# Performance work log

Hardware: AMD Instinct MI355X
Metric: run time of the kernel (lower is better)

The kernel has to match this reference:

```python
import jax, jax.numpy as jnp
import numpy as np

TMSG = 15  # max_len - 1


def setup_inputs() -> dict:
    key = jax.random.key(0)
    ks = jax.random.split(key, 8)
    B, T_in, E, H, V = 4096, 4, 256, 512, 32000
    s = lambda k, shape: jax.random.normal(k, shape, jnp.float32) * 0.05
    return {
        "inp": jax.random.normal(ks[0], (B, T_in, E), jnp.float32),
        "Wx0": s(ks[1], (E, 4 * H)),
        "Wh0": s(ks[2], (H, 4 * H)),
        "b0": jnp.zeros((4 * H,), jnp.float32),
        "Wx1": s(ks[3], (H, 4 * H)),
        "Wh1": s(ks[4], (H, 4 * H)),
        "b1": jnp.zeros((4 * H,), jnp.float32),
        "Wd": s(ks[5], (H, V)),
        "bd": jnp.zeros((V,), jnp.float32),
    }


def _lstm_step(x, h, c, Wx, Wh, b):
    # Keras LSTMCell gate order: i, f, g(cell), o
    z = x @ Wx + h @ Wh + b
    i, f, g, o = jnp.split(z, 4, axis=-1)
    c = jax.nn.sigmoid(f) * c + jax.nn.sigmoid(i) * jnp.tanh(g)
    h = jax.nn.sigmoid(o) * jnp.tanh(c)
    return h, c


def reference(inp, Wx0, Wh0, b0, Wx1, Wh1, b1, Wd, bd):
    B = inp.shape[0]
    H = Wh0.shape[0]
    z = jnp.zeros((B, H), inp.dtype)

    def scan_fn(carry, x_t):
        h0, c0, h1, c1 = carry
        h0, c0 = _lstm_step(x_t, h0, c0, Wx0, Wh0, b0)
        h1, c1 = _lstm_step(h0, h1, c1, Wx1, Wh1, b1)
        return (h0, c0, h1, c1), None

    # NOTE: source bug resets initial_state to None every step, so each of the
    # max_len-1 steps runs the identical stacked LSTM from zero state; we run it once.
    (h0, c0, h1, c1), _ = jax.lax.scan(scan_fn, (z, z, z, z), jnp.swapaxes(inp, 0, 1))
    out = h1  # (B, H) last-step output of top cell

    log_probs = jax.nn.log_softmax(out @ Wd + bd, axis=-1)  # (B, V)
    probs = jnp.exp(log_probs)
    entropy = -jnp.sum(probs * log_probs, axis=-1)  # (B,)

    keys = jax.random.split(jax.random.key(42), TMSG)
    samples = jax.vmap(lambda k: jax.random.categorical(k, log_probs, axis=-1))(keys)  # (T, B)
    lp = log_probs[jnp.arange(B)[None, :], samples]  # (T, B) log_prob of sampled chars
    ent = jnp.broadcast_to(entropy[None], (TMSG, B))  # (T, B)

    message = samples.T  # (B, T)
    message = jnp.concatenate([message, jnp.zeros_like(message)], axis=1)  # (B, 2T)
    state_h = jnp.stack([h0, c0])  # keras unpack quirk: states[0] = [h, c] of cell 0
    return (message, lp, ent, state_h)
```

## Files before the change

### kernel.cpp

```cpp
#include <hip/hip_runtime.h>
#include <stdint.h>
#include <math.h>

#define BB 4096
#define HH 512
#define VV 32000
#define NT 15
#define STF 2097152

struct KeysArg { uint32_t w[2*NT]; };

__host__ __device__ inline void tf2x32(uint32_t k0, uint32_t k1,
                                       uint32_t x0, uint32_t x1,
                                       uint32_t& o0, uint32_t& o1) {
  uint32_t ks2 = k0 ^ k1 ^ 0x1BD11BDAu;
  x0 += k0; x1 += k1;
#define TF_R(r) { x0 += x1; x1 = (x1 << (r)) | (x1 >> (32 - (r))); x1 ^= x0; }
  TF_R(13) TF_R(15) TF_R(26) TF_R(6)
  x0 += k1; x1 += ks2 + 1u;
  TF_R(17) TF_R(29) TF_R(16) TF_R(24)
  x0 += ks2; x1 += k0 + 2u;
  TF_R(13) TF_R(15) TF_R(26) TF_R(6)
  x0 += k0; x1 += k1 + 3u;
  TF_R(17) TF_R(29) TF_R(16) TF_R(24)
  x0 += k1; x1 += ks2 + 4u;
  TF_R(13) TF_R(15) TF_R(26) TF_R(6)
  x0 += ks2; x1 += k0 + 5u;
#undef TF_R
  o0 = x0; o1 = x1;
}

__device__ inline float gumbel32(uint32_t bits) {
  float f = __uint_as_float((bits >> 9) | 0x3f800000u) - 1.0f;
  f = fmaxf(f, 1.17549435e-38f);
  return -logf(-logf(f));
}

__global__ __launch_bounds__(256)
void gemm2_kernel(const float* __restrict__ A1, int lda1, int K1,
                  const float* __restrict__ A2, int lda2, int K2,
                  const float* __restrict__ W1, const float* __restrict__ W2,
                  int ldw,
                  const float* __restrict__ bias,
                  float* __restrict__ C, int ldc)
{
  __shared__ float As[16][128];
  __shared__ float Ws[16][128];
  const int tid = threadIdx.x;
  const int m0 = blockIdx.y * 128;
  const int n0 = blockIdx.x * 128;
  const int tx = tid & 15, ty = tid >> 4;
  float acc[8][8];
  #pragma unroll
  for (int i = 0; i < 8; ++i)
    #pragma unroll
    for (int j = 0; j < 8; ++j) acc[i][j] = 0.0f;

  const int kt1 = K1 >> 4;
  const int kt2 = A2 ? (K2 >> 4) : 0;
  const int sr = tid >> 1, sc = (tid & 1) * 8;
  const int wk = tid >> 4, wn = (tid & 15) * 8;

  for (int kt = 0; kt < kt1 + kt2; ++kt) {
    const float* A; int lda; const float* W; int k0;
    if (kt < kt1) { A = A1; lda = lda1; W = W1; k0 = kt << 4; }
    else          { A = A2; lda = lda2; W = W2; k0 = (kt - kt1) << 4; }
    const float* asrc = A + (size_t)(m0 + sr) * lda + (k0 + sc);
    float4 av0 = *(const float4*)asrc;
    float4 av1 = *(const float4*)(asrc + 4);
    const float* wsrc = W + (size_t)(k0 + wk) * ldw + (n0 + wn);
    float4 wv0 = *(const float4*)wsrc;
    float4 wv1 = *(const float4*)(wsrc + 4);
    As[sc+0][sr]=av0.x; As[sc+1][sr]=av0.y; As[sc+2][sr]=av0.z; As[sc+3][sr]=av0.w;
    As[sc+4][sr]=av1.x; As[sc+5][sr]=av1.y; As[sc+6][sr]=av1.z; As[sc+7][sr]=av1.w;
    *(float4*)&Ws[wk][wn]   = wv0;
    *(float4*)&Ws[wk][wn+4] = wv1;
    __syncthreads();
    #pragma unroll
    for (int kk = 0; kk < 16; ++kk) {
      float4 a0 = *(const float4*)&As[kk][ty*8];
      float4 a1 = *(const float4*)&As[kk][ty*8+4];
      float4 b0 = *(const float4*)&Ws[kk][tx*8];
      float4 b1 = *(const float4*)&Ws[kk][tx*8+4];
      float ar[8] = {a0.x,a0.y,a0.z,a0.w,a1.x,a1.y,a1.z,a1.w};
      float br[8] = {b0.x,b0.y,b0.z,b0.w,b1.x,b1.y,b1.z,b1.w};
      #pragma unroll
      for (int i = 0; i < 8; ++i)
        #pragma unroll
        for (int j = 0; j < 8; ++j)
          acc[i][j] = fmaf(ar[i], br[j], acc[i][j]);
    }
    __syncthreads();
  }
  #pragma unroll
  for (int i = 0; i < 8; ++i) {
    const int m = m0 + ty*8 + i;
    float* dst = C + (size_t)m * ldc + (n0 + tx*8);
    float4 o0, o1;
    o0.x = acc[i][0] + bias[n0+tx*8+0];
    o0.y = acc[i][1] + bias[n0+tx*8+1];
    o0.z = acc[i][2] + bias[n0+tx*8+2];
    o0.w = acc[i][3] + bias[n0+tx*8+3];
    o1.x = acc[i][4] + bias[n0+tx*8+4];
    o1.y = acc[i][5] + bias[n0+tx*8+5];
    o1.z = acc[i][6] + bias[n0+tx*8+6];
    o1.w = acc[i][7] + bias[n0+tx*8+7];
    *(float4*)dst       = o0;
    *(float4*)(dst + 4) = o1;
  }
}

__global__ __launch_bounds__(256)
void gate_kernel(const float* __restrict__ z, const float* __restrict__ cin,
                 float* __restrict__ hout, float* __restrict__ cout,
                 float* __restrict__ sh, float* __restrict__ sc)
{
  int idx = blockIdx.x * 256 + threadIdx.x;
  int b = idx >> 9, j = idx & 511;
  const float* zr = z + (size_t)b * 2048;
  float zi = zr[j], zf = zr[j+512], zg = zr[j+1024], zo = zr[j+1536];
  float si = 1.0f/(1.0f+expf(-zi));
  float sf = 1.0f/(1.0f+expf(-zf));
  float so = 1.0f/(1.0f+expf(-zo));
  float c = sf * cin[idx] + si * tanhf(zg);
  float h = so * tanhf(c);
  cout[idx] = c; hout[idx] = h;
  if (sh) { sh[idx] = h; sc[idx] = c; }
}

__global__ __launch_bounds__(256)
void rowstat_kernel(const float* __restrict__ logits,
                    float* __restrict__ rowM, float* __restrict__ rowLS,
                    float* __restrict__ rowEnt)
{
  const int row = blockIdx.x;
  const float* x = logits + (size_t)row * VV;
  const int tid = threadIdx.x;
  float m = -INFINITY;
  for (int v = tid; v < VV; v += 256) m = fmaxf(m, x[v]);
  #pragma unroll
  for (int off = 32; off; off >>= 1) m = fmaxf(m, __shfl_down(m, off));
  __shared__ float sm[4], ssum[4], swsum[4];
  if ((tid & 63) == 0) sm[tid >> 6] = m;
  __syncthreads();
  m = fmaxf(fmaxf(sm[0], sm[1]), fmaxf(sm[2], sm[3]));
  float s = 0.0f, w = 0.0f;
  for (int v = tid; v < VV; v += 256) {
    float d = x[v] - m;
    float e = expf(d);
    s += e; w += d * e;
  }
  #pragma unroll
  for (int off = 32; off; off >>= 1) { s += __shfl_down(s, off); w += __shfl_down(w, off); }
  if ((tid & 63) == 0) { ssum[tid >> 6] = s; swsum[tid >> 6] = w; }
  __syncthreads();
  if (tid == 0) {
    s = ssum[0]+ssum[1]+ssum[2]+ssum[3];
    w = swsum[0]+swsum[1]+swsum[2]+swsum[3];
    float ls = logf(s);
    rowM[row] = m; rowLS[row] = ls; rowEnt[row] = ls - w / s;
  }
}

__global__ __launch_bounds__(256)
void sample_kernel(const float* __restrict__ logits,
                   const float* __restrict__ rowM, const float* __restrict__ rowLS,
                   const float* __restrict__ rowEnt,
                   float* __restrict__ out,
                   KeysArg keys, int bbase)
{
  const int l = blockIdx.x;
  const int b = bbase + l;
  const float* x = logits + (size_t)l * VV;
  const float m = rowM[l], ls = rowLS[l];

  float bv[NT];
  uint32_t bi[NT];
  #pragma unroll
  for (int t = 0; t < NT; ++t) { bv[t] = -INFINITY; bi[t] = 0; }

  const uint32_t pbase = (uint32_t)b * (uint32_t)VV;
  for (int v = threadIdx.x; v < VV; v += 256) {
    const float lp = (x[v] - m) - ls;
    const uint32_t p = pbase + (uint32_t)v;
    #pragma unroll
    for (int t = 0; t < NT; ++t) {
      uint32_t o0, o1;
      tf2x32(keys.w[2*t], keys.w[2*t+1], 0u, p, o0, o1);
      float g = gumbel32(o0 ^ o1) + lp;
      if (g > bv[t]) { bv[t] = g; bi[t] = (uint32_t)v; }
    }
  }

  __shared__ float rv[NT][4];
  __shared__ uint32_t ri[NT][4];
  const int lane = threadIdx.x & 63, wq = threadIdx.x >> 6;
  #pragma unroll
  for (int t = 0; t < NT; ++t) {
    float v = bv[t]; uint32_t idx = bi[t];
    #pragma unroll
    for (int off = 32; off; off >>= 1) {
      float ov = __shfl_down(v, off);
      uint32_t oi = __shfl_down(idx, off);
      if (ov > v || (ov == v && oi < idx)) { v = ov; idx = oi; }
    }
    if (lane == 0) { rv[t][wq] = v; ri[t][wq] = idx; }
  }
  __syncthreads();
  if (threadIdx.x < NT) {
    const int t = threadIdx.x;
    float v = rv[t][0]; uint32_t idx = ri[t][0];
    #pragma unroll
    for (int q = 1; q < 4; ++q) {
      float ov = rv[t][q]; uint32_t oi = ri[t][q];
      if (ov > v || (ov == v && oi < idx)) { v = ov; idx = oi; }
    }
    out[(size_t)b * 30 + t]      = (float)idx;
    out[(size_t)b * 30 + 15 + t] = 0.0f;
    out[122880 + (size_t)t * BB + b] = (x[idx] - m) - ls;
    out[184320 + (size_t)t * BB + b] = rowEnt[l];
  }
}

extern "C" void kernel_launch(void* const* d_in, const int* in_sizes, int n_in,
                              void* d_out, int out_size, void* d_ws, size_t ws_size,
                              hipStream_t stream)
{
  const float* inp = (const float*)d_in[0];
  const float* Wx0 = (const float*)d_in[1];
  const float* Wh0 = (const float*)d_in[2];
  const float* b0v = (const float*)d_in[3];
  const float* Wx1 = (const float*)d_in[4];
  const float* Wh1 = (const float*)d_in[5];
  const float* b1v = (const float*)d_in[6];
  const float* Wd  = (const float*)d_in[7];
  const float* bdv = (const float*)d_in[8];
  float* out = (float*)d_out;
  float* ws = (float*)d_ws;

  float* h0 = ws;
  float* c0 = ws + (size_t)STF;
  float* h1 = ws + (size_t)2*STF;
  float* c1 = ws + (size_t)3*STF;
  float* z  = ws + (size_t)4*STF;
  float* rowM  = ws + (size_t)8*STF;
  float* rowLS = rowM + 4096;
  float* rowEnt = rowLS + 4096;
  float* logits = ws + (size_t)8*STF + 16384;

  size_t ws_floats = ws_size / 4;
  size_t base = (size_t)8*STF + 16384;
  int CH = 4096;
  while (CH > 128 && base + (size_t)CH*VV > ws_floats) CH >>= 1;

  hipMemsetAsync(ws, 0, (size_t)4*STF*sizeof(float), stream);

  for (int t = 0; t < 4; ++t) {
    gemm2_kernel<<<dim3(2048/128, 4096/128), 256, 0, stream>>>(
        inp + t*256, 1024, 256, h0, 512, 512, Wx0, Wh0, 2048, b0v, z, 2048);
    gate_kernel<<<STF/256, 256, 0, stream>>>(z, c0, h0, c0,
        (t==3) ? out + 245760 : (float*)nullptr,
        (t==3) ? out + 245760 + STF : (float*)nullptr);
    gemm2_kernel<<<dim3(2048/128, 4096/128), 256, 0, stream>>>(
        h0, 512, 512, h1, 512, 512, Wx1, Wh1, 2048, b1v, z, 2048);
    gate_kernel<<<STF/256, 256, 0, stream>>>(z, c1, h1, c1, (float*)nullptr, (float*)nullptr);
  }

  KeysArg ka;
  for (int t = 0; t < NT; ++t) {
    uint32_t o0, o1;
    tf2x32(0u, 42u, 0u, (uint32_t)t, o0, o1);
    ka.w[2*t] = o0; ka.w[2*t+1] = o1;
  }

  const int nch = 4096 / CH;
  for (int c = 0; c < nch; ++c) {
    int bbase = c * CH;
    gemm2_kernel<<<dim3(VV/128, CH/128), 256, 0, stream>>>(
        h1 + (size_t)bbase*512, 512, 512, nullptr, 0, 0, Wd, nullptr, VV, bdv,
        logits, VV);
    rowstat_kernel<<<CH, 256, 0, stream>>>(logits, rowM, rowLS, rowEnt);
    sample_kernel<<<CH, 256, 0, stream>>>(logits, rowM, rowLS, rowEnt, out, ka, bbase);
  }
}
```

Before: 8.231 ms.

## Split sampling per draw and skip Gumbel logs via running threshold bound

Each sampling block now handles one (row, draw) pair instead of all 15 draws, which raises the block count and lowers register pressure. Inside the loop, a uniform threshold derived from the current best candidate and the row log-sum-exp lets threads skip the two logarithms and the logit load when the candidate provably cannot win. Threefry bits are still generated for every element. The bound relies on log-probabilities being at most minus the log-sum-exp, and a small slack factor keeps it conservative; floating-point rounding near the threshold could in principle alter a tie.

Measured after the change: 9.583 ms. 16.4% more time.

```diff
diff --git a/kernel.cpp b/kernel.cpp
--- a/kernel.cpp
+++ b/kernel.cpp
@@ -30,12 +30,6 @@
   o0 = x0; o1 = x1;
 }
 
-__device__ inline float gumbel32(uint32_t bits) {
-  float f = __uint_as_float((bits >> 9) | 0x3f800000u) - 1.0f;
-  f = fmaxf(f, 1.17549435e-38f);
-  return -logf(-logf(f));
-}
-
 __global__ __launch_bounds__(256)
 void gemm2_kernel(const float* __restrict__ A1, int lda1, int K1,
                   const float* __restrict__ A2, int lda2, int K2,
@@ -169,50 +163,56 @@
                    float* __restrict__ out,
                    KeysArg keys, int bbase)
 {
-  const int l = blockIdx.x;
+  const int l = blockIdx.x / NT;
+  const int t = blockIdx.x % NT;
   const int b = bbase + l;
   const float* x = logits + (size_t)l * VV;
   const float m = rowM[l], ls = rowLS[l];
-
-  float bv[NT];
-  uint32_t bi[NT];
-  #pragma unroll
-  for (int t = 0; t < NT; ++t) { bv[t] = -INFINITY; bi[t] = 0; }
+  const uint32_t k0 = keys.w[2*t], k1 = keys.w[2*t+1];
+
+  float bv = -INFINITY;
+  uint32_t bi = 0;
+  float thr = 1.0f;
 
   const uint32_t pbase = (uint32_t)b * (uint32_t)VV;
   for (int v = threadIdx.x; v < VV; v += 256) {
-    const float lp = (x[v] - m) - ls;
-    const uint32_t p = pbase + (uint32_t)v;
-    #pragma unroll
-    for (int t = 0; t < NT; ++t) {
-      uint32_t o0, o1;
-      tf2x32(keys.w[2*t], keys.w[2*t+1], 0u, p, o0, o1);
-      float g = gumbel32(o0 ^ o1) + lp;
-      if (g > bv[t]) { bv[t] = g; bi[t] = (uint32_t)v; }
-    }
-  }
-
-  __shared__ float rv[NT][4];
-  __shared__ uint32_t ri[NT][4];
+    uint32_t o0, o1;
+    tf2x32(k0, k1, 0u, pbase + (uint32_t)v, o0, o1);
+    const uint32_t bits = o0 ^ o1;
+    const float uf = __uint_as_float((bits >> 9) | 0x3f800000u);
+    if (uf >= thr) {
+      float u = fmaxf(uf - 1.0f, 1.17549435e-38f);
+      float g = -logf(-logf(u));
+      float lp = (x[v] - m) - ls;
+      float cand = g + lp;
+      if (cand > bv) {
+        bv = cand; bi = (uint32_t)v;
+        float T = bv + ls;
+        float us = expf(-expf(-T));
+        thr = 1.0f + us * 0.999999f;
+      }
+    }
+  }
+
+  __shared__ float rv[4];
+  __shared__ uint32_t ri[4];
   const int lane = threadIdx.x & 63, wq = threadIdx.x >> 6;
-  #pragma unroll
-  for (int t = 0; t < NT; ++t) {
-    float v = bv[t]; uint32_t idx = bi[t];
+  {
+    float v = bv; uint32_t idx = bi;
     #pragma unroll
     for (int off = 32; off; off >>= 1) {
       float ov = __shfl_down(v, off);
       uint32_t oi = __shfl_down(idx, off);
       if (ov > v || (ov == v && oi < idx)) { v = ov; idx = oi; }
     }
-    if (lane == 0) { rv[t][wq] = v; ri[t][wq] = idx; }
+    if (lane == 0) { rv[wq] = v; ri[wq] = idx; }
   }
   __syncthreads();
-  if (threadIdx.x < NT) {
-    const int t = threadIdx.x;
-    float v = rv[t][0]; uint32_t idx = ri[t][0];
+  if (threadIdx.x == 0) {
+    float v = rv[0]; uint32_t idx = ri[0];
     #pragma unroll
     for (int q = 1; q < 4; ++q) {
-      float ov = rv[t][q]; uint32_t oi = ri[t][q];
+      float ov = rv[q]; uint32_t oi = ri[q];
       if (ov > v || (ov == v && oi < idx)) { v = ov; idx = oi; }
     }
     out[(size_t)b * 30 + t]      = (float)idx;
@@ -280,6 +280,6 @@
         h1 + (size_t)bbase*512, 512, 512, nullptr, 0, 0, Wd, nullptr, VV, bdv,
         logits, VV);
     rowstat_kernel<<<CH, 256, 0, stream>>>(logits, rowM, rowLS, rowEnt);
-    sample_kernel<<<CH, 256, 0, stream>>>(logits, rowM, rowLS, rowEnt, out, ka, bbase);
-  }
-}
+    sample_kernel<<<CH * NT, 256, 0, stream>>>(logits, rowM, rowLS, rowEnt, out, ka, bbase);
+  }
+}
```

## Hoist input projection, split-K recurrent GEMMs across grid z, interleave W columns

Applied to the files above, without the earlier changes.

Computes the layer-0 input projection for all four timesteps in one large GEMM before the recurrence. Each recurrent GEMM is split into two K halves run as separate grid-z slices that write partial sums to z0 and z1, which the gate kernel adds together with the bias. This doubles the number of blocks per launch to improve occupancy. The W tile column mapping changes from 8 contiguous columns per thread to two groups of 4 spaced 64 apart, meant to reduce LDS bank conflicts. The cost is extra partial-sum traffic, and the workspace is reused for z buffers that alias the logits region.

After: 8.274 ms. No clear change (+0.5%).

```diff
diff --git a/kernel.cpp b/kernel.cpp
--- a/kernel.cpp
+++ b/kernel.cpp
@@ -30,20 +30,19 @@
   o0 = x0; o1 = x1;
 }
 
-__device__ inline float gumbel32(uint32_t bits) {
-  float f = __uint_as_float((bits >> 9) | 0x3f800000u) - 1.0f;
-  f = fmaxf(f, 1.17549435e-38f);
-  return -logf(-logf(f));
-}
-
 __global__ __launch_bounds__(256)
-void gemm2_kernel(const float* __restrict__ A1, int lda1, int K1,
-                  const float* __restrict__ A2, int lda2, int K2,
-                  const float* __restrict__ W1, const float* __restrict__ W2,
-                  int ldw,
-                  const float* __restrict__ bias,
-                  float* __restrict__ C, int ldc)
-{
+void gemm_sk(const float* __restrict__ A0, int lda0,
+             const float* __restrict__ W0, int koff0,
+             const float* __restrict__ A1, int lda1,
+             const float* __restrict__ W1, int koff1,
+             int ldw, int Klen,
+             const float* __restrict__ bias,
+             float* __restrict__ C0, float* __restrict__ C1, int ldc)
+{
+  const float* A; const float* W; float* C; int lda, koff;
+  if (blockIdx.z == 0) { A = A0; lda = lda0; W = W0; koff = koff0; C = C0; }
+  else                 { A = A1; lda = lda1; W = W1; koff = koff1; C = C1; }
+
   __shared__ float As[16][128];
   __shared__ float Ws[16][128];
   const int tid = threadIdx.x;
@@ -56,32 +55,29 @@
     #pragma unroll
     for (int j = 0; j < 8; ++j) acc[i][j] = 0.0f;
 
-  const int kt1 = K1 >> 4;
-  const int kt2 = A2 ? (K2 >> 4) : 0;
   const int sr = tid >> 1, sc = (tid & 1) * 8;
-  const int wk = tid >> 4, wn = (tid & 15) * 8;
-
-  for (int kt = 0; kt < kt1 + kt2; ++kt) {
-    const float* A; int lda; const float* W; int k0;
-    if (kt < kt1) { A = A1; lda = lda1; W = W1; k0 = kt << 4; }
-    else          { A = A2; lda = lda2; W = W2; k0 = (kt - kt1) << 4; }
+  const int wk = tid >> 4, wn = (tid & 15) * 4;
+
+  const int nkt = Klen >> 4;
+  for (int kt = 0; kt < nkt; ++kt) {
+    const int k0 = koff + (kt << 4);
     const float* asrc = A + (size_t)(m0 + sr) * lda + (k0 + sc);
     float4 av0 = *(const float4*)asrc;
     float4 av1 = *(const float4*)(asrc + 4);
     const float* wsrc = W + (size_t)(k0 + wk) * ldw + (n0 + wn);
     float4 wv0 = *(const float4*)wsrc;
-    float4 wv1 = *(const float4*)(wsrc + 4);
+    float4 wv1 = *(const float4*)(wsrc + 64);
     As[sc+0][sr]=av0.x; As[sc+1][sr]=av0.y; As[sc+2][sr]=av0.z; As[sc+3][sr]=av0.w;
     As[sc+4][sr]=av1.x; As[sc+5][sr]=av1.y; As[sc+6][sr]=av1.z; As[sc+7][sr]=av1.w;
-    *(float4*)&Ws[wk][wn]   = wv0;
-    *(float4*)&Ws[wk][wn+4] = wv1;
+    *(float4*)&Ws[wk][wn]      = wv0;
+    *(float4*)&Ws[wk][wn + 64] = wv1;
     __syncthreads();
     #pragma unroll
     for (int kk = 0; kk < 16; ++kk) {
       float4 a0 = *(const float4*)&As[kk][ty*8];
       float4 a1 = *(const float4*)&As[kk][ty*8+4];
-      float4 b0 = *(const float4*)&Ws[kk][tx*8];
-      float4 b1 = *(const float4*)&Ws[kk][tx*8+4];
+      float4 b0 = *(const float4*)&Ws[kk][tx*4];
+      float4 b1 = *(const float4*)&Ws[kk][tx*4+64];
       float ar[8] = {a0.x,a0.y,a0.z,a0.w,a1.x,a1.y,a1.z,a1.w};
       float br[8] = {b0.x,b0.y,b0.z,b0.w,b1.x,b1.y,b1.z,b1.w};
       #pragma unroll
@@ -92,33 +88,45 @@
     }
     __syncthreads();
   }
+
   #pragma unroll
   for (int i = 0; i < 8; ++i) {
     const int m = m0 + ty*8 + i;
-    float* dst = C + (size_t)m * ldc + (n0 + tx*8);
+    float* dst = C + (size_t)m * ldc + (n0 + wn);
     float4 o0, o1;
-    o0.x = acc[i][0] + bias[n0+tx*8+0];
-    o0.y = acc[i][1] + bias[n0+tx*8+1];
-    o0.z = acc[i][2] + bias[n0+tx*8+2];
-    o0.w = acc[i][3] + bias[n0+tx*8+3];
-    o1.x = acc[i][4] + bias[n0+tx*8+4];
-    o1.y = acc[i][5] + bias[n0+tx*8+5];
-    o1.z = acc[i][6] + bias[n0+tx*8+6];
-    o1.w = acc[i][7] + bias[n0+tx*8+7];
-    *(float4*)dst       = o0;
-    *(float4*)(dst + 4) = o1;
+    o0.x = acc[i][0]; o0.y = acc[i][1]; o0.z = acc[i][2]; o0.w = acc[i][3];
+    o1.x = acc[i][4]; o1.y = acc[i][5]; o1.z = acc[i][6]; o1.w = acc[i][7];
+    if (bias) {
+      o0.x += bias[n0+wn+0]; o0.y += bias[n0+wn+1];
+      o0.z += bias[n0+wn+2]; o0.w += bias[n0+wn+3];
+      o1.x += bias[n0+wn+64]; o1.y += bias[n0+wn+65];
+      o1.z += bias[n0+wn+66]; o1.w += bias[n0+wn+67];
+    }
+    *(float4*)dst        = o0;
+    *(float4*)(dst + 64) = o1;
   }
 }
 
 __global__ __launch_bounds__(256)
-void gate_kernel(const float* __restrict__ z, const float* __restrict__ cin,
+void gate_kernel(const float* __restrict__ zx, int zxs,
+                 const float* __restrict__ z0, const float* __restrict__ z1,
+                 const float* __restrict__ bias,
+                 const float* __restrict__ cin,
                  float* __restrict__ hout, float* __restrict__ cout,
                  float* __restrict__ sh, float* __restrict__ sc)
 {
   int idx = blockIdx.x * 256 + threadIdx.x;
   int b = idx >> 9, j = idx & 511;
-  const float* zr = z + (size_t)b * 2048;
-  float zi = zr[j], zf = zr[j+512], zg = zr[j+1024], zo = zr[j+1536];
+  const size_t r2 = (size_t)b * 2048;
+  float zi, zf, zg, zo;
+  zi = z0[r2+j]      + z1[r2+j]      + bias[j];
+  zf = z0[r2+j+512]  + z1[r2+j+512]  + bias[j+512];
+  zg = z0[r2+j+1024] + z1[r2+j+1024] + bias[j+1024];
+  zo = z0[r2+j+1536] + z1[r2+j+1536] + bias[j+1536];
+  if (zx) {
+    const size_t rx = (size_t)b * zxs;
+    zi += zx[rx+j]; zf += zx[rx+j+512]; zg += zx[rx+j+1024]; zo += zx[rx+j+1536];
+  }
   float si = 1.0f/(1.0f+expf(-zi));
   float sf = 1.0f/(1.0f+expf(-zf));
   float so = 1.0f/(1.0f+expf(-zo));
@@ -187,7 +195,10 @@
     for (int t = 0; t < NT; ++t) {
       uint32_t o0, o1;
       tf2x32(keys.w[2*t], keys.w[2*t+1], 0u, p, o0, o1);
-      float g = gumbel32(o0 ^ o1) + lp;
+      const uint32_t bits = o0 ^ o1;
+      float u = fmaxf(__uint_as_float((bits >> 9) | 0x3f800000u) - 1.0f,
+                      1.17549435e-38f);
+      float g = -logf(-logf(u)) + lp;
       if (g > bv[t]) { bv[t] = g; bi[t] = (uint32_t)v; }
     }
   }
@@ -242,28 +253,38 @@
   float* c0 = ws + (size_t)STF;
   float* h1 = ws + (size_t)2*STF;
   float* c1 = ws + (size_t)3*STF;
-  float* z  = ws + (size_t)4*STF;
-  float* rowM  = ws + (size_t)8*STF;
+  float* rowM  = ws + (size_t)4*STF;
   float* rowLS = rowM + 4096;
   float* rowEnt = rowLS + 4096;
-  float* logits = ws + (size_t)8*STF + 16384;
+  float* logits = ws + (size_t)4*STF + 12288;
+  float* zxpre = logits;
+  float* z0 = zxpre + (size_t)16384*2048;
+  float* z1 = z0 + (size_t)4096*2048;
 
   size_t ws_floats = ws_size / 4;
-  size_t base = (size_t)8*STF + 16384;
+  size_t base = (size_t)4*STF + 12288;
   int CH = 4096;
   while (CH > 128 && base + (size_t)CH*VV > ws_floats) CH >>= 1;
 
   hipMemsetAsync(ws, 0, (size_t)4*STF*sizeof(float), stream);
 
+  gemm_sk<<<dim3(2048/128, 16384/128, 1), 256, 0, stream>>>(
+      inp, 256, Wx0, 0,  nullptr, 0, nullptr, 0,
+      2048, 256, nullptr, zxpre, nullptr, 2048);
+
   for (int t = 0; t < 4; ++t) {
-    gemm2_kernel<<<dim3(2048/128, 4096/128), 256, 0, stream>>>(
-        inp + t*256, 1024, 256, h0, 512, 512, Wx0, Wh0, 2048, b0v, z, 2048);
-    gate_kernel<<<STF/256, 256, 0, stream>>>(z, c0, h0, c0,
+    gemm_sk<<<dim3(2048/128, 4096/128, 2), 256, 0, stream>>>(
+        h0, 512, Wh0, 0,  h0, 512, Wh0, 256,
+        2048, 256, nullptr, z0, z1, 2048);
+    gate_kernel<<<STF/256, 256, 0, stream>>>(
+        zxpre + t*2048, 8192, z0, z1, b0v, c0, h0, c0,
         (t==3) ? out + 245760 : (float*)nullptr,
         (t==3) ? out + 245760 + STF : (float*)nullptr);
-    gemm2_kernel<<<dim3(2048/128, 4096/128), 256, 0, stream>>>(
-        h0, 512, 512, h1, 512, 512, Wx1, Wh1, 2048, b1v, z, 2048);
-    gate_kernel<<<STF/256, 256, 0, stream>>>(z, c1, h1, c1, (float*)nullptr, (float*)nullptr);
+    gemm_sk<<<dim3(2048/128, 4096/128, 2), 256, 0, stream>>>(
+        h0, 512, Wx1, 0,  h1, 512, Wh1, 0,
+        2048, 512, nullptr, z0, z1, 2048);
+    gate_kernel<<<STF/256, 256, 0, stream>>>(
+        nullptr, 0, z0, z1, b1v, c1, h1, c1, (float*)nullptr, (float*)nullptr);
   }
 
   KeysArg ka;
@@ -276,9 +297,9 @@
   const int nch = 4096 / CH;
   for (int c = 0; c < nch; ++c) {
     int bbase = c * CH;
-    gemm2_kernel<<<dim3(VV/128, CH/128), 256, 0, stream>>>(
-        h1 + (size_t)bbase*512, 512, 512, nullptr, 0, 0, Wd, nullptr, VV, bdv,
-        logits, VV);
+    gemm_sk<<<dim3(VV/128, CH/128, 1), 256, 0, stream>>>(
+        h1 + (size_t)bbase*512, 512, Wd, 0,  nullptr, 0, nullptr, 0,
+        VV, 512, bdv, logits, nullptr, VV);
     rowstat_kernel<<<CH, 256, 0, stream>>>(logits, rowM, rowLS, rowEnt);
     sample_kernel<<<CH, 256, 0, stream>>>(logits, rowM, rowLS, rowEnt, out, ka, bbase);
   }
```
